# Kernel tuning notes

Measured on AMD Instinct MI355X. Metric: run time of the kernel, lower is better.

The kernel has to match this reference:

```python
import jax, jax.numpy as jnp
import numpy as np


def setup_inputs() -> dict:
    key = jax.random.key(0)
    kq, kk, kv = jax.random.split(key, 3)
    B, H, S, D = 2, 8, 2048, 64
    Q = jax.random.normal(kq, (B, H, S, D), dtype=jnp.float32)
    K = jax.random.normal(kk, (B, 1, S, D), dtype=jnp.float32)
    V = jax.random.normal(kv, (B, 1, S, D), dtype=jnp.float32)
    return {"Q": Q, "K": K, "V": V}


def reference(Q, K, V):
    # Multi-query attention: K/V have a single shared head.
    D = Q.shape[-1]
    scale = 1.0 / jnp.sqrt(jnp.asarray(D, dtype=Q.dtype))
    Kh = K[:, 0]  # [B, S, D]
    Vh = V[:, 0]  # [B, S, D]
    # scores: [B, H, Sq, Sk]
    scores = jnp.einsum('bhqd,bkd->bhqk', Q, Kh) * scale
    probs = jax.nn.softmax(scores, axis=-1)
    out = jnp.einsum('bhqk,bkd->bhqd', probs, Vh)  # [B, H, S, D]
    return out
```

## Files before the change

kernel.cpp:

```cpp
#include <hip/hip_runtime.h>
#include <hip/hip_bf16.h>
#include <stdint.h>

typedef __attribute__((ext_vector_type(8)))  short    bf16x8;
typedef __attribute__((ext_vector_type(16))) float    f32x16;
typedef __attribute__((ext_vector_type(2)))  float    f32x2;
typedef __attribute__((ext_vector_type(4)))  float    float4v;
typedef __attribute__((ext_vector_type(4)))  unsigned uint4v;
typedef __attribute__((ext_vector_type(2)))  int      int2v;

#define DEVINL static __device__ __forceinline__

#define B_  2
#define H_  8
#define S_  2048
#define D_  64
#define KVB 128
#define NKT (S_ / KVB)

DEVINL unsigned short f2bf(float f) {
  union { float f; unsigned u; } v; v.f = f;
  unsigned r = v.u + 0x7FFFu + ((v.u >> 16) & 1u);
  return (unsigned short)(r >> 16);
}

DEVINL unsigned short bfu(float f) {
  __hip_bfloat16 h = __float2bfloat16(f);
  unsigned short u; __builtin_memcpy(&u, &h, 2); return u;
}

DEVINL unsigned pkcvt(float a, float b) {
  return (unsigned)bfu(a) | ((unsigned)bfu(b) << 16);
}

DEVINL void gload_lds16(const void* g, void* l) {
  __builtin_amdgcn_global_load_lds(
      (const __attribute__((address_space(1))) void*)g,
      (__attribute__((address_space(3))) void*)l, 16, 0, 0);
}

DEVINL bf16x8 frag_from_words(unsigned a, unsigned b, unsigned c, unsigned d) {
  union { unsigned u[4]; bf16x8 v; } x;
  x.u[0] = a; x.u[1] = b; x.u[2] = c; x.u[3] = d;
  return x.v;
}

#define CROW(r, hi) (((r) & 3) + 8 * ((r) >> 2) + 4 * (hi))

__global__ __launch_bounds__(256) void prep_kernel(
    const float* __restrict__ K, const float* __restrict__ V,
    unsigned short* __restrict__ KVf) {
  const int blk = blockIdx.x;
  const int b  = blk >> 5;
  const int kt = (blk >> 1) & 15;
  const int t  = threadIdx.x;
  const int w  = t >> 6, l = t & 63;
  const int lq = l & 31, hi = l >> 5;

  unsigned short* out = KVf + (size_t)(b * 16 + kt) * 16384;

  if ((blk & 1) == 0) {
#pragma unroll
    for (int j = 0; j < 4; ++j) {
      const int fi = w * 4 + j;
      const int kh = fi >> 2, ks = fi & 3;
      const float* src = K + ((size_t)(b * 2048 + kt * 128 + kh * 32 + lq)) * 64 + ks * 16 + hi * 8;
      const float4v x0 = *(const float4v*)(src);
      const float4v x1 = *(const float4v*)(src + 4);
      uint4v o;
      o.x = (unsigned)f2bf(x0.x) | ((unsigned)f2bf(x0.y) << 16);
      o.y = (unsigned)f2bf(x0.z) | ((unsigned)f2bf(x0.w) << 16);
      o.z = (unsigned)f2bf(x1.x) | ((unsigned)f2bf(x1.y) << 16);
      o.w = (unsigned)f2bf(x1.z) | ((unsigned)f2bf(x1.w) << 16);
      *(uint4v*)(out + fi * 512 + l * 8) = o;
    }
  } else {
    __shared__ float Vs[128][65];
#pragma unroll
    for (int rep = 0; rep < 4; ++rep) {
      const int row = rep * 32 + (t >> 3);
      const int col = (t & 7) * 8;
      const float* src = V + ((size_t)(b * 2048 + kt * 128 + row)) * 64 + col;
      const float4v y0 = *(const float4v*)(src);
      const float4v y1 = *(const float4v*)(src + 4);
      Vs[row][col + 0] = y0.x; Vs[row][col + 1] = y0.y;
      Vs[row][col + 2] = y0.z; Vs[row][col + 3] = y0.w;
      Vs[row][col + 4] = y1.x; Vs[row][col + 5] = y1.y;
      Vs[row][col + 6] = y1.z; Vs[row][col + 7] = y1.w;
    }
    __syncthreads();
#pragma unroll
    for (int j = 0; j < 4; ++j) {
      const int fj = w * 4 + j;
      const int kh = fj >> 2, s = (fj >> 1) & 1, nt = fj & 1;
      const int d  = nt * 32 + lq;
      const int k0 = kh * 32 + s * 16 + hi * 8;
      unsigned short o[8];
#pragma unroll
      for (int e = 0; e < 8; ++e) o[e] = f2bf(Vs[k0 + e][d]);
      uint4v wv;
      wv.x = (unsigned)o[0] | ((unsigned)o[1] << 16);
      wv.y = (unsigned)o[2] | ((unsigned)o[3] << 16);
      wv.z = (unsigned)o[4] | ((unsigned)o[5] << 16);
      wv.w = (unsigned)o[6] | ((unsigned)o[7] << 16);
      *(uint4v*)(out + (16 + fj) * 512 + l * 8) = wv;
    }
  }
}

__global__ __launch_bounds__(256, 4) void attn_kernel(
    const float* __restrict__ Q, const unsigned short* __restrict__ KVf,
    float* __restrict__ O) {
  __shared__ __align__(16) unsigned char smem[32768];

  const int bid = blockIdx.x;
  const int b  = bid >> 9;
  const int h  = (bid >> 6) & 7;
  const int qt = bid & 63;

  const int tid  = threadIdx.x;
  const int lane = tid & 63;
  const int kh   = tid >> 6;
  const int hi   = lane >> 5;
  const int lq   = lane & 31;

  const unsigned char* ksrc = (const unsigned char*)KVf
      + (size_t)b * 524288 + (size_t)kh * 4096 + (size_t)lane * 16;
  const unsigned char* vp = ksrc + 16384;
  unsigned char* wdst = smem + (size_t)kh * 4096 + (size_t)lane * 16;

  const float qscale = 0.125f * 1.4426950408889634f;
  const float* qrow = Q + ((size_t)((b * H_ + h) * S_) + (size_t)(qt * 32 + lq)) * 64;
  bf16x8 qfrag[4];
#pragma unroll
  for (int ks = 0; ks < 4; ++ks) {
    const float* p = qrow + ks * 16 + hi * 8;
    float4v x0 = *(const float4v*)(p);
    float4v x1 = *(const float4v*)(p + 4);
    bf16x8 f;
    f[0] = (short)f2bf(x0.x * qscale); f[1] = (short)f2bf(x0.y * qscale);
    f[2] = (short)f2bf(x0.z * qscale); f[3] = (short)f2bf(x0.w * qscale);
    f[4] = (short)f2bf(x1.x * qscale); f[5] = (short)f2bf(x1.y * qscale);
    f[6] = (short)f2bf(x1.z * qscale); f[7] = (short)f2bf(x1.w * qscale);
    qfrag[ks] = f;
  }

  f32x16 acc0, acc1;
#pragma unroll
  for (int r = 0; r < 16; ++r) { acc0[r] = 0.f; acc1[r] = 0.f; }
  float lrun = 0.f;

#pragma unroll
  for (int j = 0; j < 4; ++j) gload_lds16(ksrc + j * 1024, wdst + j * 1024);
  const unsigned char* kp = ksrc + 32768;

  int buf = 0;
  for (int kt = 0; kt < NKT; ++kt) {
    const bf16x8 v0 = *(const bf16x8*)(vp);
    const bf16x8 v1 = *(const bf16x8*)(vp + 1024);
    const bf16x8 v2 = *(const bf16x8*)(vp + 2048);
    const bf16x8 v3 = *(const bf16x8*)(vp + 3072);
    vp += 32768;

    asm volatile("s_waitcnt vmcnt(4)" ::: "memory");
    __builtin_amdgcn_sched_barrier(0);

    if (kt + 1 < NKT) {
#pragma unroll
      for (int j = 0; j < 4; ++j)
        gload_lds16(kp + j * 1024, smem + (buf ^ 1) * 16384 + kh * 4096 + lane * 16 + j * 1024);
      kp += 32768;
    }

    const unsigned short* Kt = (const unsigned short*)(smem + buf * 16384 + kh * 4096);
    f32x16 c;
#pragma unroll
    for (int r = 0; r < 16; ++r) c[r] = 0.f;
    __builtin_amdgcn_s_setprio(1);
#pragma unroll
    for (int ks = 0; ks < 4; ++ks) {
      const bf16x8 a = *(const bf16x8*)(Kt + ks * 512 + lane * 8);
      c = __builtin_amdgcn_mfma_f32_32x32x16_bf16(a, qfrag[ks], c, 0, 0, 0);
    }
    __builtin_amdgcn_s_setprio(0);

#pragma unroll
    for (int r = 0; r < 16; ++r) c[r] = __builtin_amdgcn_exp2f(c[r]);
    f32x2 ps = (f32x2){0.f, 0.f};
#pragma unroll
    for (int r = 0; r < 8; ++r) ps += (f32x2){c[2 * r], c[2 * r + 1]};
    lrun += ps.x + ps.y;

    const unsigned wa0 = pkcvt(c[0], c[1]),   wa1 = pkcvt(c[2], c[3]);
    const unsigned wa2 = pkcvt(c[4], c[5]),   wa3 = pkcvt(c[6], c[7]);
    const unsigned wb0 = pkcvt(c[8], c[9]),   wb1 = pkcvt(c[10], c[11]);
    const unsigned wb2 = pkcvt(c[12], c[13]), wb3 = pkcvt(c[14], c[15]);
    const int2v a02 = __builtin_amdgcn_permlane32_swap((int)wa0, (int)wa2, false, false);
    const int2v a13 = __builtin_amdgcn_permlane32_swap((int)wa1, (int)wa3, false, false);
    const int2v b02 = __builtin_amdgcn_permlane32_swap((int)wb0, (int)wb2, false, false);
    const int2v b13 = __builtin_amdgcn_permlane32_swap((int)wb1, (int)wb3, false, false);
    const bf16x8 pf0 = frag_from_words((unsigned)a02.x, (unsigned)a13.x,
                                       (unsigned)a02.y, (unsigned)a13.y);
    const bf16x8 pf1 = frag_from_words((unsigned)b02.x, (unsigned)b13.x,
                                       (unsigned)b02.y, (unsigned)b13.y);

    __builtin_amdgcn_s_setprio(1);
    acc0 = __builtin_amdgcn_mfma_f32_32x32x16_bf16(pf0, v0, acc0, 0, 0, 0);
    acc1 = __builtin_amdgcn_mfma_f32_32x32x16_bf16(pf0, v1, acc1, 0, 0, 0);
    acc0 = __builtin_amdgcn_mfma_f32_32x32x16_bf16(pf1, v2, acc0, 0, 0, 0);
    acc1 = __builtin_amdgcn_mfma_f32_32x32x16_bf16(pf1, v3, acc1, 0, 0, 0);
    __builtin_amdgcn_s_setprio(0);

    buf ^= 1;
  }

  const float lfull = lrun + __shfl_xor(lrun, 32);
  __syncthreads();
  float* Lb = (float*)smem;
  float* Ab = Lb + 128;
  if (lane < 32) Lb[kh * 32 + lane] = lfull;
  if (kh > 0) {
    float* dst = Ab + (size_t)(kh - 1) * 2048;
#pragma unroll
    for (int r = 0; r < 16; ++r) {
      const int row = CROW(r, hi);
      dst[row * 64 + lq]      = acc0[r];
      dst[row * 64 + 32 + lq] = acc1[r];
    }
  }
  __syncthreads();
  if (kh == 0) {
    const float ltot = Lb[lq] + Lb[32 + lq] + Lb[64 + lq] + Lb[96 + lq];
    const float linv = 1.f / ltot;
    float* obase = O + ((size_t)((b * H_ + h) * S_) + (size_t)(qt * 32)) * 64;
#pragma unroll
    for (int r = 0; r < 16; ++r) {
      const int row = CROW(r, hi);
      const float iv = __shfl(linv, row);
      const float* A = Ab + row * 64;
      obase[(size_t)row * 64 + lq] =
          (acc0[r] + A[lq] + A[2048 + lq] + A[4096 + lq]) * iv;
      obase[(size_t)row * 64 + 32 + lq] =
          (acc1[r] + A[32 + lq] + A[2048 + 32 + lq] + A[4096 + 32 + lq]) * iv;
    }
  }
}

extern "C" void kernel_launch(void* const* d_in, const int* in_sizes, int n_in,
                              void* d_out, int out_size, void* d_ws, size_t ws_size,
                              hipStream_t stream) {
  const float* Q = (const float*)d_in[0];
  const float* K = (const float*)d_in[1];
  const float* V = (const float*)d_in[2];
  float* O = (float*)d_out;

  unsigned short* KVf = (unsigned short*)d_ws;

  prep_kernel<<<64, 256, 0, stream>>>(K, V, KVf);
  attn_kernel<<<B_ * H_ * (S_ / 32), 256, 0, stream>>>(Q, KVf, O);
}
```

Measured before the change: 40.15 us.

## Load K directly from global into registers and interleave two KV tiles per iteration

Replaces the LDS double-buffered K staging (global_load_lds with waitcnt) with direct global-to-register loads of K and V fragments, processing two independent KV tiles per loop iteration so their QK MFMA chains and softmax/PV steps interleave. This removes the LDS round-trip and its wait synchronization, relying on two independent chains for latency hiding. Shared memory shrinks to just the epilogue reduction buffer, and launch bounds drop from 4 to 3 blocks per CU to allow more registers per thread. The trade-off is higher register pressure and lower occupancy, with global load latency exposed unless the compiler schedules the loads early.

New measurement: 38.93 us. 1.03x faster.

```diff
diff --git a/kernel.cpp b/kernel.cpp
--- a/kernel.cpp
+++ b/kernel.cpp
@@ -15,8 +15,6 @@
 #define H_  8
 #define S_  2048
 #define D_  64
-#define KVB 128
-#define NKT (S_ / KVB)
 
 DEVINL unsigned short f2bf(float f) {
   union { float f; unsigned u; } v; v.f = f;
@@ -31,12 +29,6 @@
 
 DEVINL unsigned pkcvt(float a, float b) {
   return (unsigned)bfu(a) | ((unsigned)bfu(b) << 16);
-}
-
-DEVINL void gload_lds16(const void* g, void* l) {
-  __builtin_amdgcn_global_load_lds(
-      (const __attribute__((address_space(1))) void*)g,
-      (__attribute__((address_space(3))) void*)l, 16, 0, 0);
 }
 
 DEVINL bf16x8 frag_from_words(unsigned a, unsigned b, unsigned c, unsigned d) {
@@ -108,10 +100,48 @@
   }
 }
 
-__global__ __launch_bounds__(256, 4) void attn_kernel(
+#define CHAIN_QK(Cc, K0, K1, K2, K3)                                                   \
+  do {                                                                                 \
+    __builtin_amdgcn_s_setprio(1);                                                     \
+    Cc = __builtin_amdgcn_mfma_f32_32x32x16_bf16(K0, qfrag[0], Cc, 0, 0, 0);           \
+    Cc = __builtin_amdgcn_mfma_f32_32x32x16_bf16(K1, qfrag[1], Cc, 0, 0, 0);           \
+    Cc = __builtin_amdgcn_mfma_f32_32x32x16_bf16(K2, qfrag[2], Cc, 0, 0, 0);           \
+    Cc = __builtin_amdgcn_mfma_f32_32x32x16_bf16(K3, qfrag[3], Cc, 0, 0, 0);           \
+    __builtin_amdgcn_s_setprio(0);                                                     \
+  } while (0)
+
+#define CHAIN_FIN(Cc, V0, V1, V2, V3)                                                  \
+  do {                                                                                 \
+    _Pragma("unroll") for (int r = 0; r < 16; ++r)                                     \
+      Cc[r] = __builtin_amdgcn_exp2f(Cc[r]);                                           \
+    f32x2 ps = (f32x2){0.f, 0.f};                                                      \
+    _Pragma("unroll") for (int r = 0; r < 8; ++r)                                      \
+      ps += (f32x2){Cc[2 * r], Cc[2 * r + 1]};                                         \
+    lrun += ps.x + ps.y;                                                               \
+    const unsigned wa0 = pkcvt(Cc[0], Cc[1]),   wa1 = pkcvt(Cc[2], Cc[3]);             \
+    const unsigned wa2 = pkcvt(Cc[4], Cc[5]),   wa3 = pkcvt(Cc[6], Cc[7]);             \
+    const unsigned wb0 = pkcvt(Cc[8], Cc[9]),   wb1 = pkcvt(Cc[10], Cc[11]);           \
+    const unsigned wb2 = pkcvt(Cc[12], Cc[13]), wb3 = pkcvt(Cc[14], Cc[15]);           \
+    const int2v a02 = __builtin_amdgcn_permlane32_swap((int)wa0, (int)wa2, false, false); \
+    const int2v a13 = __builtin_amdgcn_permlane32_swap((int)wa1, (int)wa3, false, false); \
+    const int2v b02 = __builtin_amdgcn_permlane32_swap((int)wb0, (int)wb2, false, false); \
+    const int2v b13 = __builtin_amdgcn_permlane32_swap((int)wb1, (int)wb3, false, false); \
+    const bf16x8 pf0 = frag_from_words((unsigned)a02.x, (unsigned)a13.x,               \
+                                       (unsigned)a02.y, (unsigned)a13.y);              \
+    const bf16x8 pf1 = frag_from_words((unsigned)b02.x, (unsigned)b13.x,               \
+                                       (unsigned)b02.y, (unsigned)b13.y);              \
+    __builtin_amdgcn_s_setprio(1);                                                     \
+    acc0 = __builtin_amdgcn_mfma_f32_32x32x16_bf16(pf0, V0, acc0, 0, 0, 0);            \
+    acc1 = __builtin_amdgcn_mfma_f32_32x32x16_bf16(pf0, V1, acc1, 0, 0, 0);            \
+    acc0 = __builtin_amdgcn_mfma_f32_32x32x16_bf16(pf1, V2, acc0, 0, 0, 0);            \
+    acc1 = __builtin_amdgcn_mfma_f32_32x32x16_bf16(pf1, V3, acc1, 0, 0, 0);            \
+    __builtin_amdgcn_s_setprio(0);                                                     \
+  } while (0)
+
+__global__ __launch_bounds__(256, 3) void attn_kernel(
     const float* __restrict__ Q, const unsigned short* __restrict__ KVf,
     float* __restrict__ O) {
-  __shared__ __align__(16) unsigned char smem[32768];
+  __shared__ __align__(16) float smem_f[6400];
 
   const int bid = blockIdx.x;
   const int b  = bid >> 9;
@@ -124,10 +154,8 @@
   const int hi   = lane >> 5;
   const int lq   = lane & 31;
 
-  const unsigned char* ksrc = (const unsigned char*)KVf
+  const unsigned char* base = (const unsigned char*)KVf
       + (size_t)b * 524288 + (size_t)kh * 4096 + (size_t)lane * 16;
-  const unsigned char* vp = ksrc + 16384;
-  unsigned char* wdst = smem + (size_t)kh * 4096 + (size_t)lane * 16;
 
   const float qscale = 0.125f * 1.4426950408889634f;
   const float* qrow = Q + ((size_t)((b * H_ + h) * S_) + (size_t)(qt * 32 + lq)) * 64;
@@ -150,74 +178,45 @@
   for (int r = 0; r < 16; ++r) { acc0[r] = 0.f; acc1[r] = 0.f; }
   float lrun = 0.f;
 
-#pragma unroll
-  for (int j = 0; j < 4; ++j) gload_lds16(ksrc + j * 1024, wdst + j * 1024);
-  const unsigned char* kp = ksrc + 32768;
-
-  int buf = 0;
-  for (int kt = 0; kt < NKT; ++kt) {
-    const bf16x8 v0 = *(const bf16x8*)(vp);
-    const bf16x8 v1 = *(const bf16x8*)(vp + 1024);
-    const bf16x8 v2 = *(const bf16x8*)(vp + 2048);
-    const bf16x8 v3 = *(const bf16x8*)(vp + 3072);
-    vp += 32768;
-
-    asm volatile("s_waitcnt vmcnt(4)" ::: "memory");
-    __builtin_amdgcn_sched_barrier(0);
-
-    if (kt + 1 < NKT) {
-#pragma unroll
-      for (int j = 0; j < 4; ++j)
-        gload_lds16(kp + j * 1024, smem + (buf ^ 1) * 16384 + kh * 4096 + lane * 16 + j * 1024);
-      kp += 32768;
-    }
-
-    const unsigned short* Kt = (const unsigned short*)(smem + buf * 16384 + kh * 4096);
-    f32x16 c;
-#pragma unroll
-    for (int r = 0; r < 16; ++r) c[r] = 0.f;
-    __builtin_amdgcn_s_setprio(1);
-#pragma unroll
-    for (int ks = 0; ks < 4; ++ks) {
-      const bf16x8 a = *(const bf16x8*)(Kt + ks * 512 + lane * 8);
-      c = __builtin_amdgcn_mfma_f32_32x32x16_bf16(a, qfrag[ks], c, 0, 0, 0);
-    }
-    __builtin_amdgcn_s_setprio(0);
-
-#pragma unroll
-    for (int r = 0; r < 16; ++r) c[r] = __builtin_amdgcn_exp2f(c[r]);
-    f32x2 ps = (f32x2){0.f, 0.f};
-#pragma unroll
-    for (int r = 0; r < 8; ++r) ps += (f32x2){c[2 * r], c[2 * r + 1]};
-    lrun += ps.x + ps.y;
-
-    const unsigned wa0 = pkcvt(c[0], c[1]),   wa1 = pkcvt(c[2], c[3]);
-    const unsigned wa2 = pkcvt(c[4], c[5]),   wa3 = pkcvt(c[6], c[7]);
-    const unsigned wb0 = pkcvt(c[8], c[9]),   wb1 = pkcvt(c[10], c[11]);
-    const unsigned wb2 = pkcvt(c[12], c[13]), wb3 = pkcvt(c[14], c[15]);
-    const int2v a02 = __builtin_amdgcn_permlane32_swap((int)wa0, (int)wa2, false, false);
-    const int2v a13 = __builtin_amdgcn_permlane32_swap((int)wa1, (int)wa3, false, false);
-    const int2v b02 = __builtin_amdgcn_permlane32_swap((int)wb0, (int)wb2, false, false);
-    const int2v b13 = __builtin_amdgcn_permlane32_swap((int)wb1, (int)wb3, false, false);
-    const bf16x8 pf0 = frag_from_words((unsigned)a02.x, (unsigned)a13.x,
-                                       (unsigned)a02.y, (unsigned)a13.y);
-    const bf16x8 pf1 = frag_from_words((unsigned)b02.x, (unsigned)b13.x,
-                                       (unsigned)b02.y, (unsigned)b13.y);
-
-    __builtin_amdgcn_s_setprio(1);
-    acc0 = __builtin_amdgcn_mfma_f32_32x32x16_bf16(pf0, v0, acc0, 0, 0, 0);
-    acc1 = __builtin_amdgcn_mfma_f32_32x32x16_bf16(pf0, v1, acc1, 0, 0, 0);
-    acc0 = __builtin_amdgcn_mfma_f32_32x32x16_bf16(pf1, v2, acc0, 0, 0, 0);
-    acc1 = __builtin_amdgcn_mfma_f32_32x32x16_bf16(pf1, v3, acc1, 0, 0, 0);
-    __builtin_amdgcn_s_setprio(0);
-
-    buf ^= 1;
+  const unsigned char* pA = base;
+  const unsigned char* pB = base + 32768;
+
+  for (int it = 0; it < 8; ++it) {
+    const bf16x8 kA0 = *(const bf16x8*)(pA);
+    const bf16x8 kA1 = *(const bf16x8*)(pA + 1024);
+    const bf16x8 kA2 = *(const bf16x8*)(pA + 2048);
+    const bf16x8 kA3 = *(const bf16x8*)(pA + 3072);
+    const bf16x8 kB0 = *(const bf16x8*)(pB);
+    const bf16x8 kB1 = *(const bf16x8*)(pB + 1024);
+    const bf16x8 kB2 = *(const bf16x8*)(pB + 2048);
+    const bf16x8 kB3 = *(const bf16x8*)(pB + 3072);
+
+    f32x16 cA, cB;
+#pragma unroll
+    for (int r = 0; r < 16; ++r) { cA[r] = 0.f; cB[r] = 0.f; }
+    CHAIN_QK(cA, kA0, kA1, kA2, kA3);
+    CHAIN_QK(cB, kB0, kB1, kB2, kB3);
+
+    const bf16x8 vA0 = *(const bf16x8*)(pA + 16384);
+    const bf16x8 vA1 = *(const bf16x8*)(pA + 17408);
+    const bf16x8 vA2 = *(const bf16x8*)(pA + 18432);
+    const bf16x8 vA3 = *(const bf16x8*)(pA + 19456);
+    const bf16x8 vB0 = *(const bf16x8*)(pB + 16384);
+    const bf16x8 vB1 = *(const bf16x8*)(pB + 17408);
+    const bf16x8 vB2 = *(const bf16x8*)(pB + 18432);
+    const bf16x8 vB3 = *(const bf16x8*)(pB + 19456);
+
+    CHAIN_FIN(cA, vA0, vA1, vA2, vA3);
+    CHAIN_FIN(cB, vB0, vB1, vB2, vB3);
+
+    pA += 65536;
+    pB += 65536;
   }
 
   const float lfull = lrun + __shfl_xor(lrun, 32);
   __syncthreads();
-  float* Lb = (float*)smem;
-  float* Ab = Lb + 128;
+  float* Lb = smem_f;
+  float* Ab = smem_f + 128;
   if (lane < 32) Lb[kh * 32 + lane] = lfull;
   if (kh > 0) {
     float* dst = Ab + (size_t)(kh - 1) * 2048;
```
